# Kernel optimization log

Measured on AMD Instinct MI355X. Metric: run time of the kernel, lower is better.

## Reference

```python
import jax, jax.numpy as jnp
import numpy as np

N_HEADS = 16
N_CHANNELS = 1024
DIM_HEAD = N_CHANNELS // N_HEADS


def setup_inputs() -> dict:
    key = jax.random.key(0)
    k1, k2, k3, k4 = jax.random.split(key, 4)
    B, S, D = 4, 2048, N_CHANNELS
    x = jax.random.normal(k1, (B, S, D), dtype=jnp.float32)
    # in_proj: Linear(D, 3D, bias=False); torch weight shape [3D, D], y = x @ W.T
    w_in = jax.random.normal(k2, (3 * D, D), dtype=jnp.float32) * (1.0 / np.sqrt(D))
    # out_proj: Linear(D, D) with bias
    w_out = jax.random.normal(k3, (D, D), dtype=jnp.float32) * (1.0 / np.sqrt(D))
    b_out = jax.random.normal(k4, (D,), dtype=jnp.float32) * 0.01
    return {"x": x, "w_in": w_in, "w_out": w_out, "b_out": b_out}


def reference(x, w_in, w_out, b_out):
    B, S, D = x.shape
    H, Dh = N_HEADS, DIM_HEAD
    qkv = jnp.einsum('bsd,ed->bse', x, w_in)  # [B,S,3D]
    q, k, v = jnp.split(qkv, 3, axis=-1)
    # [B,S,D] -> [B,H,S,Dh]
    def to_heads(t):
        return t.reshape(B, S, H, Dh).transpose(0, 2, 1, 3)
    q, k, v = to_heads(q), to_heads(k), to_heads(v)
    scale = 1.0 / np.sqrt(Dh)
    scores = jnp.einsum('bhqd,bhkd->bhqk', q, k) * scale  # [B,H,S,S]
    attn = jax.nn.softmax(scores, axis=-1)
    out = jnp.einsum('bhqk,bhkd->bhqd', attn, v)  # [B,H,S,Dh]
    out = out.transpose(0, 2, 1, 3).reshape(B, S, D)
    return jnp.einsum('bsd,ed->bse', out, w_out) + b_out
```

## Files before the change

### kernel.cpp

```cpp
#include <hip/hip_runtime.h>

typedef __bf16 bf16;
typedef __bf16 bf16x2 __attribute__((ext_vector_type(2)));
typedef __bf16 bf16x4 __attribute__((ext_vector_type(4)));
typedef __bf16 bf16x8 __attribute__((ext_vector_type(8)));
typedef float f32x4 __attribute__((ext_vector_type(4)));

typedef __attribute__((address_space(1))) const unsigned int gq_t;
typedef __attribute__((address_space(3))) unsigned int lq_t;

__global__ __launch_bounds__(256) void cvt_bf16(const float* __restrict__ in,
                                                bf16* __restrict__ out,
                                                int n8) {
  int i = blockIdx.x * 256 + threadIdx.x;
  if (i >= n8) return;
  f32x4 a = ((const f32x4*)in)[2 * i];
  f32x4 b = ((const f32x4*)in)[2 * i + 1];
  bf16x8 o;
#pragma unroll
  for (int j = 0; j < 4; ++j) {
    o[j] = (bf16)a[j];
    o[4 + j] = (bf16)b[j];
  }
  ((bf16x8*)out)[i] = o;
}

template <typename TC, bool ADD_BIAS>
__global__ __launch_bounds__(256) void gemm_glds(const bf16* __restrict__ A,
                                                 const bf16* __restrict__ B,
                                                 const float* __restrict__ bias,
                                                 TC* __restrict__ C,
                                                 int M, int N, int K, int lda) {
  __shared__ __align__(16) bf16 As[128 * 64];
  __shared__ __align__(16) bf16 Bs[128 * 64];
  const int tid = threadIdx.x;
  const int lane = tid & 63;
  const int wid = tid >> 6;
  const int wr = wid >> 1, wc = wid & 1;
  const int m0 = blockIdx.y * 128;
  const int n0 = blockIdx.x * 128;
  const int l16 = lane & 15;
  const int lhi = lane >> 4;
  const int lr = lane >> 3;
  const int lc = (lane & 7) * 8;

  f32x4 acc[4][4] = {};

  for (int k0 = 0; k0 < K; k0 += 64) {
    __syncthreads();
#pragma unroll
    for (int i = 0; i < 4; ++i) {
      const int chunk = wid * 4 + i;
      const int row = chunk * 8 + lr;
      const bf16* ga = A + (size_t)(m0 + row) * lda + k0 + lc;
      const bf16* gb = B + (size_t)(n0 + row) * K + k0 + lc;
      __builtin_amdgcn_global_load_lds((gq_t*)ga, (lq_t*)&As[chunk * 512], 16,
                                       0, 0);
      __builtin_amdgcn_global_load_lds((gq_t*)gb, (lq_t*)&Bs[chunk * 512], 16,
                                       0, 0);
    }
    __syncthreads();
#pragma unroll
    for (int ks = 0; ks < 2; ++ks) {
      bf16x8 af[4], bfr[4];
#pragma unroll
      for (int i = 0; i < 4; ++i) {
        af[i] = *(const bf16x8*)(&As[(wr * 64 + i * 16 + l16) * 64 + ks * 32 +
                                     lhi * 8]);
        bfr[i] = *(const bf16x8*)(&Bs[(wc * 64 + i * 16 + l16) * 64 + ks * 32 +
                                      lhi * 8]);
      }
#pragma unroll
      for (int i = 0; i < 4; ++i)
#pragma unroll
        for (int j = 0; j < 4; ++j)
          acc[i][j] = __builtin_amdgcn_mfma_f32_16x16x32_bf16(af[i], bfr[j],
                                                              acc[i][j], 0, 0, 0);
    }
  }

#pragma unroll
  for (int i = 0; i < 4; ++i) {
    int row_base = m0 + wr * 64 + i * 16 + lhi * 4;
#pragma unroll
    for (int j = 0; j < 4; ++j) {
      int col = n0 + wc * 64 + j * 16 + l16;
      float bv = ADD_BIAS ? bias[col] : 0.0f;
#pragma unroll
      for (int r = 0; r < 4; ++r) {
        float val = acc[i][j][r] + bv;
        if constexpr (__is_same(TC, float))
          C[(size_t)(row_base + r) * N + col] = val;
        else
          C[(size_t)(row_base + r) * N + col] = (bf16)val;
      }
    }
  }
}

template <typename TA, typename TC, bool ADD_BIAS>
__global__ __launch_bounds__(256) void gemm_bt(const TA* __restrict__ A,
                                               const float* __restrict__ B,
                                               const float* __restrict__ bias,
                                               TC* __restrict__ C,
                                               int M, int N, int K,
                                               int lda, int row0) {
  __shared__ __align__(16) bf16 As[128][72];
  __shared__ __align__(16) bf16 Bs[128][72];
  const int tid = threadIdx.x;
  const int lane = tid & 63;
  const int wid = tid >> 6;
  const int wr = wid >> 1, wc = wid & 1;
  const int m0 = blockIdx.y * 128;
  const int n0 = blockIdx.x * 128;
  const int l16 = lane & 15;
  const int lhi = lane >> 4;

  f32x4 acc[4][4] = {};

  for (int k0 = 0; k0 < K; k0 += 64) {
    __syncthreads();
#pragma unroll
    for (int p = 0; p < 8; ++p) {
      int v = tid + p * 256;
      int row = v >> 4;
      int kc = (v & 15) * 4;
      size_t ai = (size_t)(row0 + m0 + row) * lda + k0 + kc;
      size_t bi = (size_t)(n0 + row) * K + k0 + kc;
      bf16x4 ab, bb;
      if constexpr (__is_same(TA, float)) {
        f32x4 a4 = *(const f32x4*)((const float*)A + ai);
#pragma unroll
        for (int j = 0; j < 4; ++j) ab[j] = (bf16)a4[j];
      } else {
        ab = *(const bf16x4*)((const bf16*)A + ai);
      }
      f32x4 b4 = *(const f32x4*)(B + bi);
#pragma unroll
      for (int j = 0; j < 4; ++j) bb[j] = (bf16)b4[j];
      *(bf16x4*)(&As[row][kc]) = ab;
      *(bf16x4*)(&Bs[row][kc]) = bb;
    }
    __syncthreads();
#pragma unroll
    for (int ks = 0; ks < 2; ++ks) {
      bf16x8 af[4], bfr[4];
#pragma unroll
      for (int i = 0; i < 4; ++i) {
        af[i] = *(const bf16x8*)(&As[wr * 64 + i * 16 + l16][ks * 32 + lhi * 8]);
        bfr[i] = *(const bf16x8*)(&Bs[wc * 64 + i * 16 + l16][ks * 32 + lhi * 8]);
      }
#pragma unroll
      for (int i = 0; i < 4; ++i)
#pragma unroll
        for (int j = 0; j < 4; ++j)
          acc[i][j] = __builtin_amdgcn_mfma_f32_16x16x32_bf16(af[i], bfr[j],
                                                              acc[i][j], 0, 0, 0);
    }
  }

#pragma unroll
  for (int i = 0; i < 4; ++i) {
    int row_base = m0 + wr * 64 + i * 16 + lhi * 4;
#pragma unroll
    for (int j = 0; j < 4; ++j) {
      int col = n0 + wc * 64 + j * 16 + l16;
      float bv = ADD_BIAS ? bias[col] : 0.0f;
#pragma unroll
      for (int r = 0; r < 4; ++r) {
        float val = acc[i][j][r] + bv;
        if constexpr (__is_same(TC, float))
          C[(size_t)(row_base + r) * N + col] = val;
        else
          C[(size_t)(row_base + r) * N + col] = (bf16)val;
      }
    }
  }
}

__global__ __launch_bounds__(256) void attn_fwd(bf16* __restrict__ qkv) {
  constexpr int S = 2048, D3 = 3072;
  constexpr float SCL = 0.18033688011112042f;
  constexpr float THR = 11.5f;
  __shared__ __align__(16) bf16 Kt[2][64][72];
  __shared__ __align__(16) bf16 Vt[2][64][72];
  __shared__ __align__(16) bf16 Pq[4][16][72];

  const int tid = threadIdx.x;
  const int lane = tid & 63;
  const int wid = tid >> 6;
  const int l16 = lane & 15, lhi = lane >> 4;

  const int nwg = gridDim.x * gridDim.y;
  const int bid = blockIdx.y * 32 + blockIdx.x;
  const int swz = (bid & 7) * (nwg >> 3) + (bid >> 3);
  const int bh = swz >> 5;
  const int b = bh >> 4, h = bh & 15;
  const int q0 = (swz & 31) * 64 + wid * 16;

  bf16* base = qkv + (size_t)b * S * D3;
  bf16* qbase = base + h * 64;
  const bf16* kbase = base + 1024 + h * 64;
  const bf16* vbase = base + 2048 + h * 64;

  bf16x8 qf[2];
#pragma unroll
  for (int ks = 0; ks < 2; ++ks)
    qf[ks] = *(const bf16x8*)(qbase + (size_t)(q0 + l16) * D3 + ks * 32 + lhi * 8);

  float m_i = -1e30f;
  float l_part = 0.0f;
  f32x4 o[4] = {};

  const int kp = tid & 31, oc = tid >> 5;

  {
    bf16x8 k0 = *(const bf16x8*)(kbase + (size_t)(2 * kp) * D3 + oc * 8);
    bf16x8 k1 = *(const bf16x8*)(kbase + (size_t)(2 * kp + 1) * D3 + oc * 8);
    bf16x8 v0 = *(const bf16x8*)(vbase + (size_t)(2 * kp) * D3 + oc * 8);
    bf16x8 v1 = *(const bf16x8*)(vbase + (size_t)(2 * kp + 1) * D3 + oc * 8);
    *(bf16x8*)(&Kt[0][2 * kp][oc * 8]) = k0;
    *(bf16x8*)(&Kt[0][2 * kp + 1][oc * 8]) = k1;
#pragma unroll
    for (int j = 0; j < 8; ++j) {
      bf16x2 pr;
      pr[0] = v0[j];
      pr[1] = v1[j];
      *(bf16x2*)(&Vt[0][oc * 8 + j][2 * kp]) = pr;
    }
  }
  __syncthreads();

  for (int t = 0; t < S; t += 64) {
    const int cur = (t >> 6) & 1;
    const bool havenext = (t + 64 < S);

    bf16x8 kn0, kn1, vn0, vn1;
    if (havenext) {
      const bf16* kb = kbase + (size_t)(t + 64) * D3;
      const bf16* vb = vbase + (size_t)(t + 64) * D3;
      kn0 = *(const bf16x8*)(kb + (size_t)(2 * kp) * D3 + oc * 8);
      kn1 = *(const bf16x8*)(kb + (size_t)(2 * kp + 1) * D3 + oc * 8);
      vn0 = *(const bf16x8*)(vb + (size_t)(2 * kp) * D3 + oc * 8);
      vn1 = *(const bf16x8*)(vb + (size_t)(2 * kp + 1) * D3 + oc * 8);
    }

    f32x4 sc[4] = {};
    __builtin_amdgcn_s_setprio(1);
#pragma unroll
    for (int ct = 0; ct < 4; ++ct) {
#pragma unroll
      for (int ks = 0; ks < 2; ++ks) {
        bf16x8 kf = *(const bf16x8*)(&Kt[cur][ct * 16 + l16][ks * 32 + lhi * 8]);
        sc[ct] = __builtin_amdgcn_mfma_f32_16x16x32_bf16(kf, qf[ks], sc[ct], 0, 0, 0);
      }
    }
    __builtin_amdgcn_s_setprio(0);

    float cm[4];
#pragma unroll
    for (int ct = 0; ct < 4; ++ct)
      cm[ct] = fmaxf(fmaxf(sc[ct][0], sc[ct][1]), fmaxf(sc[ct][2], sc[ct][3]));
    float mxs = fmaxf(fmaxf(cm[0], cm[1]), fmaxf(cm[2], cm[3])) * SCL;

    if (!__all(mxs - m_i <= THR)) {
      float mw = mxs;
      mw = fmaxf(mw, __shfl_xor(mw, 16));
      mw = fmaxf(mw, __shfl_xor(mw, 32));
      float nm = fmaxf(m_i, mw);
      float alpha = __builtin_amdgcn_exp2f(m_i - nm);
      m_i = nm;
      l_part *= alpha;
#pragma unroll
      for (int dt = 0; dt < 4; ++dt)
#pragma unroll
        for (int r = 0; r < 4; ++r) o[dt][r] *= alpha;
    }

    if (havenext) {
      *(bf16x8*)(&Kt[cur ^ 1][2 * kp][oc * 8]) = kn0;
      *(bf16x8*)(&Kt[cur ^ 1][2 * kp + 1][oc * 8]) = kn1;
#pragma unroll
      for (int j = 0; j < 8; ++j) {
        bf16x2 pr;
        pr[0] = vn0[j];
        pr[1] = vn1[j];
        *(bf16x2*)(&Vt[cur ^ 1][oc * 8 + j][2 * kp]) = pr;
      }
    }

    float rs4[4];
#pragma unroll
    for (int ct = 0; ct < 4; ++ct) {
#pragma unroll
      for (int r = 0; r < 4; ++r) {
        float p = __builtin_amdgcn_exp2f(__builtin_fmaf(sc[ct][r], SCL, -m_i));
        sc[ct][r] = p;
      }
      rs4[ct] = (sc[ct][0] + sc[ct][1]) + (sc[ct][2] + sc[ct][3]);
    }
    l_part += (rs4[0] + rs4[1]) + (rs4[2] + rs4[3]);

#pragma unroll
    for (int ct = 0; ct < 4; ++ct) {
      bf16x4 pk;
#pragma unroll
      for (int r = 0; r < 4; ++r) pk[r] = (bf16)sc[ct][r];
      *(bf16x4*)(&Pq[wid][l16][ct * 16 + lhi * 4]) = pk;
    }
    bf16x8 pf0 = *(const bf16x8*)(&Pq[wid][l16][lhi * 8]);
    bf16x8 pf1 = *(const bf16x8*)(&Pq[wid][l16][32 + lhi * 8]);

    __builtin_amdgcn_s_setprio(1);
#pragma unroll
    for (int dt = 0; dt < 4; ++dt) {
      bf16x8 vf0 = *(const bf16x8*)(&Vt[cur][dt * 16 + l16][lhi * 8]);
      bf16x8 vf1 = *(const bf16x8*)(&Vt[cur][dt * 16 + l16][32 + lhi * 8]);
      o[dt] = __builtin_amdgcn_mfma_f32_16x16x32_bf16(vf0, pf0, o[dt], 0, 0, 0);
      o[dt] = __builtin_amdgcn_mfma_f32_16x16x32_bf16(vf1, pf1, o[dt], 0, 0, 0);
    }
    __builtin_amdgcn_s_setprio(0);

    __syncthreads();
  }

  float l_i = l_part;
  l_i += __shfl_xor(l_i, 16);
  l_i += __shfl_xor(l_i, 32);
  float rl = 1.0f / l_i;
#pragma unroll
  for (int dt = 0; dt < 4; ++dt) {
    bf16x4 ok;
#pragma unroll
    for (int r = 0; r < 4; ++r) ok[r] = (bf16)(o[dt][r] * rl);
    *(bf16x4*)(&Pq[wid][l16][dt * 16 + lhi * 4]) = ok;
  }
  bf16x8 r0 = *(const bf16x8*)(&Pq[wid][l16][lhi * 16]);
  bf16x8 r1 = *(const bf16x8*)(&Pq[wid][l16][lhi * 16 + 8]);
  bf16* orow = qbase + (size_t)(q0 + l16) * D3 + lhi * 16;
  *(bf16x8*)(orow) = r0;
  *(bf16x8*)(orow + 8) = r1;
}

extern "C" void kernel_launch(void* const* d_in, const int* in_sizes, int n_in,
                              void* d_out, int out_size, void* d_ws,
                              size_t ws_size, hipStream_t stream) {
  constexpr int B = 4, S = 2048, D = 1024;

  const float* x = nullptr;
  const float* w_in = nullptr;
  const float* w_out = nullptr;
  const float* b_out = nullptr;
  for (int i = 0; i < n_in; ++i) {
    switch (in_sizes[i]) {
      case 8388608: x = (const float*)d_in[i]; break;
      case 3145728: w_in = (const float*)d_in[i]; break;
      case 1048576: w_out = (const float*)d_in[i]; break;
      case 1024: b_out = (const float*)d_in[i]; break;
    }
  }
  float* out = (float*)d_out;

  bf16* qkv = (bf16*)d_ws;
  const size_t need_full = (size_t)B * S * 3 * D * 2;
  const size_t need_cvt = need_full +
                          ((size_t)B * S * D +
                           (size_t)3 * D * D +
                           (size_t)D * D) * 2;

  if (ws_size >= need_cvt) {
    bf16* xb = qkv + (size_t)B * S * 3 * D;
    bf16* w_inb = xb + (size_t)B * S * D;
    bf16* w_outb = w_inb + (size_t)3 * D * D;
    const int nx8 = B * S * D / 8;
    const int nwi8 = 3 * D * D / 8;
    const int nwo8 = D * D / 8;
    cvt_bf16<<<dim3((nx8 + 255) / 256), 256, 0, stream>>>(x, xb, nx8);
    cvt_bf16<<<dim3((nwi8 + 255) / 256), 256, 0, stream>>>(w_in, w_inb, nwi8);
    cvt_bf16<<<dim3((nwo8 + 255) / 256), 256, 0, stream>>>(w_out, w_outb, nwo8);

    gemm_glds<bf16, false><<<dim3(3 * D / 128, B * S / 128), 256, 0, stream>>>(
        xb, w_inb, nullptr, qkv, B * S, 3 * D, D, D);
    attn_fwd<<<dim3(S / 64, B * 16), 256, 0, stream>>>(qkv);
    gemm_glds<float, true><<<dim3(D / 128, B * S / 128), 256, 0, stream>>>(
        qkv, w_outb, b_out, out, B * S, D, D, 3 * D);
  } else if (ws_size >= need_full) {
    gemm_bt<float, bf16, false><<<dim3(3 * D / 128, B * S / 128), 256, 0,
                                  stream>>>(x, w_in, nullptr, qkv, B * S,
                                            3 * D, D, D, 0);
    attn_fwd<<<dim3(S / 64, B * 16), 256, 0, stream>>>(qkv);
    gemm_bt<bf16, float, true><<<dim3(D / 128, B * S / 128), 256, 0, stream>>>(
        qkv, w_out, b_out, out, B * S, D, D, 3 * D, 0);
  } else {
    for (int b0 = 0; b0 < B; ++b0) {
      gemm_bt<float, bf16, false><<<dim3(3 * D / 128, S / 128), 256, 0,
                                    stream>>>(x, w_in, nullptr, qkv, S, 3 * D,
                                              D, D, b0 * S);
      attn_fwd<<<dim3(S / 64, 16), 256, 0, stream>>>(qkv);
      gemm_bt<bf16, float, true><<<dim3(D / 128, S / 128), 256, 0, stream>>>(
          qkv, w_out, b_out, out + (size_t)b0 * S * D, S, D, D, 3 * D, 0);
    }
  }
}
```

Baseline: 356.1 us.

## Process two 16-row query tiles per wave in attention to reuse K/V tiles

Each wave now handles 32 query rows (two independent 16-row tiles with separate softmax state), so each workgroup covers 128 queries and the grid is halved. K and V tiles loaded into shared memory, and the K/V fragments read from it, are reused across twice as many queries, cutting global and LDS traffic per query. In exchange it roughly doubles accumulator and score registers, which may lower occupancy, and halves the number of workgroups (1024 instead of 2048).

```diff
diff --git a/kernel.cpp b/kernel.cpp
--- a/kernel.cpp
+++ b/kernel.cpp
@@ -192,25 +192,27 @@
   const int l16 = lane & 15, lhi = lane >> 4;
 
   const int nwg = gridDim.x * gridDim.y;
-  const int bid = blockIdx.y * 32 + blockIdx.x;
+  const int bid = blockIdx.y * gridDim.x + blockIdx.x;
   const int swz = (bid & 7) * (nwg >> 3) + (bid >> 3);
-  const int bh = swz >> 5;
+  const int bh = swz >> 4;
   const int b = bh >> 4, h = bh & 15;
-  const int q0 = (swz & 31) * 64 + wid * 16;
+  const int q0 = (swz & 15) * 128 + wid * 32;
 
   bf16* base = qkv + (size_t)b * S * D3;
   bf16* qbase = base + h * 64;
   const bf16* kbase = base + 1024 + h * 64;
   const bf16* vbase = base + 2048 + h * 64;
 
-  bf16x8 qf[2];
-#pragma unroll
-  for (int ks = 0; ks < 2; ++ks)
-    qf[ks] = *(const bf16x8*)(qbase + (size_t)(q0 + l16) * D3 + ks * 32 + lhi * 8);
-
-  float m_i = -1e30f;
-  float l_part = 0.0f;
-  f32x4 o[4] = {};
+  bf16x8 qfA[2], qfB[2];
+#pragma unroll
+  for (int ks = 0; ks < 2; ++ks) {
+    qfA[ks] = *(const bf16x8*)(qbase + (size_t)(q0 + l16) * D3 + ks * 32 + lhi * 8);
+    qfB[ks] = *(const bf16x8*)(qbase + (size_t)(q0 + 16 + l16) * D3 + ks * 32 + lhi * 8);
+  }
+
+  float mA = -1e30f, mB = -1e30f;
+  float lA = 0.0f, lB = 0.0f;
+  f32x4 oA[4] = {}, oB[4] = {};
 
   const int kp = tid & 31, oc = tid >> 5;
 
@@ -245,37 +247,100 @@
       vn1 = *(const bf16x8*)(vb + (size_t)(2 * kp + 1) * D3 + oc * 8);
     }
 
-    f32x4 sc[4] = {};
+    f32x4 scA[4] = {}, scB[4] = {};
     __builtin_amdgcn_s_setprio(1);
 #pragma unroll
     for (int ct = 0; ct < 4; ++ct) {
 #pragma unroll
       for (int ks = 0; ks < 2; ++ks) {
         bf16x8 kf = *(const bf16x8*)(&Kt[cur][ct * 16 + l16][ks * 32 + lhi * 8]);
-        sc[ct] = __builtin_amdgcn_mfma_f32_16x16x32_bf16(kf, qf[ks], sc[ct], 0, 0, 0);
+        scA[ct] = __builtin_amdgcn_mfma_f32_16x16x32_bf16(kf, qfA[ks], scA[ct], 0, 0, 0);
+        scB[ct] = __builtin_amdgcn_mfma_f32_16x16x32_bf16(kf, qfB[ks], scB[ct], 0, 0, 0);
       }
     }
     __builtin_amdgcn_s_setprio(0);
 
-    float cm[4];
-#pragma unroll
-    for (int ct = 0; ct < 4; ++ct)
-      cm[ct] = fmaxf(fmaxf(sc[ct][0], sc[ct][1]), fmaxf(sc[ct][2], sc[ct][3]));
-    float mxs = fmaxf(fmaxf(cm[0], cm[1]), fmaxf(cm[2], cm[3])) * SCL;
-
-    if (!__all(mxs - m_i <= THR)) {
-      float mw = mxs;
-      mw = fmaxf(mw, __shfl_xor(mw, 16));
-      mw = fmaxf(mw, __shfl_xor(mw, 32));
-      float nm = fmaxf(m_i, mw);
-      float alpha = __builtin_amdgcn_exp2f(m_i - nm);
-      m_i = nm;
-      l_part *= alpha;
-#pragma unroll
-      for (int dt = 0; dt < 4; ++dt)
-#pragma unroll
-        for (int r = 0; r < 4; ++r) o[dt][r] *= alpha;
-    }
+    {
+      float cm[4];
+#pragma unroll
+      for (int ct = 0; ct < 4; ++ct)
+        cm[ct] = fmaxf(fmaxf(scA[ct][0], scA[ct][1]), fmaxf(scA[ct][2], scA[ct][3]));
+      float mxs = fmaxf(fmaxf(cm[0], cm[1]), fmaxf(cm[2], cm[3])) * SCL;
+      if (!__all(mxs - mA <= THR)) {
+        float mw = mxs;
+        mw = fmaxf(mw, __shfl_xor(mw, 16));
+        mw = fmaxf(mw, __shfl_xor(mw, 32));
+        float nm = fmaxf(mA, mw);
+        float alpha = __builtin_amdgcn_exp2f(mA - nm);
+        mA = nm;
+        lA *= alpha;
+#pragma unroll
+        for (int dt = 0; dt < 4; ++dt)
+#pragma unroll
+          for (int r = 0; r < 4; ++r) oA[dt][r] *= alpha;
+      }
+      float rs4[4];
+#pragma unroll
+      for (int ct = 0; ct < 4; ++ct) {
+#pragma unroll
+        for (int r = 0; r < 4; ++r) {
+          float p = __builtin_amdgcn_exp2f(__builtin_fmaf(scA[ct][r], SCL, -mA));
+          scA[ct][r] = p;
+        }
+        rs4[ct] = (scA[ct][0] + scA[ct][1]) + (scA[ct][2] + scA[ct][3]);
+      }
+      lA += (rs4[0] + rs4[1]) + (rs4[2] + rs4[3]);
+    }
+#pragma unroll
+    for (int ct = 0; ct < 4; ++ct) {
+      bf16x4 pk;
+#pragma unroll
+      for (int r = 0; r < 4; ++r) pk[r] = (bf16)scA[ct][r];
+      *(bf16x4*)(&Pq[wid][l16][ct * 16 + lhi * 4]) = pk;
+    }
+    bf16x8 pfA0 = *(const bf16x8*)(&Pq[wid][l16][lhi * 8]);
+    bf16x8 pfA1 = *(const bf16x8*)(&Pq[wid][l16][32 + lhi * 8]);
+
+    {
+      float cm[4];
+#pragma unroll
+      for (int ct = 0; ct < 4; ++ct)
+        cm[ct] = fmaxf(fmaxf(scB[ct][0], scB[ct][1]), fmaxf(scB[ct][2], scB[ct][3]));
+      float mxs = fmaxf(fmaxf(cm[0], cm[1]), fmaxf(cm[2], cm[3])) * SCL;
+      if (!__all(mxs - mB <= THR)) {
+        float mw = mxs;
+        mw = fmaxf(mw, __shfl_xor(mw, 16));
+        mw = fmaxf(mw, __shfl_xor(mw, 32));
+        float nm = fmaxf(mB, mw);
+        float alpha = __builtin_amdgcn_exp2f(mB - nm);
+        mB = nm;
+        lB *= alpha;
+#pragma unroll
+        for (int dt = 0; dt < 4; ++dt)
+#pragma unroll
+          for (int r = 0; r < 4; ++r) oB[dt][r] *= alpha;
+      }
+      float rs4[4];
+#pragma unroll
+      for (int ct = 0; ct < 4; ++ct) {
+#pragma unroll
+        for (int r = 0; r < 4; ++r) {
+          float p = __builtin_amdgcn_exp2f(__builtin_fmaf(scB[ct][r], SCL, -mB));
+          scB[ct][r] = p;
+        }
+        rs4[ct] = (scB[ct][0] + scB[ct][1]) + (scB[ct][2] + scB[ct][3]);
+      }
+      lB += (rs4[0] + rs4[1]) + (rs4[2] + rs4[3]);
+    }
+#pragma unroll
+    for (int ct = 0; ct < 4; ++ct) {
+      bf16x4 pk;
+#pragma unroll
+      for (int r = 0; r < 4; ++r) pk[r] = (bf16)scB[ct][r];
+      *(bf16x4*)(&Pq[wid][l16][ct * 16 + lhi * 4]) = pk;
+    }
+    bf16x8 pfB0 = *(const bf16x8*)(&Pq[wid][l16][lhi * 8]);
+    bf16x8 pfB1 = *(const bf16x8*)(&Pq[wid][l16][32 + lhi * 8]);
 
     if (havenext) {
       *(bf16x8*)(&Kt[cur ^ 1][2 * kp][oc * 8]) = kn0;
@@ -289,57 +354,57 @@
       }
     }
 
-    float rs4[4];
-#pragma unroll
-    for (int ct = 0; ct < 4; ++ct) {
-#pragma unroll
-      for (int r = 0; r < 4; ++r) {
-        float p = __builtin_amdgcn_exp2f(__builtin_fmaf(sc[ct][r], SCL, -m_i));
-        sc[ct][r] = p;
-      }
-      rs4[ct] = (sc[ct][0] + sc[ct][1]) + (sc[ct][2] + sc[ct][3]);
-    }
-    l_part += (rs4[0] + rs4[1]) + (rs4[2] + rs4[3]);
-
-#pragma unroll
-    for (int ct = 0; ct < 4; ++ct) {
-      bf16x4 pk;
-#pragma unroll
-      for (int r = 0; r < 4; ++r) pk[r] = (bf16)sc[ct][r];
-      *(bf16x4*)(&Pq[wid][l16][ct * 16 + lhi * 4]) = pk;
-    }
-    bf16x8 pf0 = *(const bf16x8*)(&Pq[wid][l16][lhi * 8]);
-    bf16x8 pf1 = *(const bf16x8*)(&Pq[wid][l16][32 + lhi * 8]);
-
     __builtin_amdgcn_s_setprio(1);
 #pragma unroll
     for (int dt = 0; dt < 4; ++dt) {
       bf16x8 vf0 = *(const bf16x8*)(&Vt[cur][dt * 16 + l16][lhi * 8]);
       bf16x8 vf1 = *(const bf16x8*)(&Vt[cur][dt * 16 + l16][32 + lhi * 8]);
-      o[dt] = __builtin_amdgcn_mfma_f32_16x16x32_bf16(vf0, pf0, o[dt], 0, 0, 0);
-      o[dt] = __builtin_amdgcn_mfma_f32_16x16x32_bf16(vf1, pf1, o[dt], 0, 0, 0);
+      oA[dt] = __builtin_amdgcn_mfma_f32_16x16x32_bf16(vf0, pfA0, oA[dt], 0, 0, 0);
+      oA[dt] = __builtin_amdgcn_mfma_f32_16x16x32_bf16(vf1, pfA1, oA[dt], 0, 0, 0);
+      oB[dt] = __builtin_amdgcn_mfma_f32_16x16x32_bf16(vf0, pfB0, oB[dt], 0, 0, 0);
+      oB[dt] = __builtin_amdgcn_mfma_f32_16x16x32_bf16(vf1, pfB1, oB[dt], 0, 0, 0);
     }
     __builtin_amdgcn_s_setprio(0);
 
     __syncthreads();
   }
 
-  float l_i = l_part;
-  l_i += __shfl_xor(l_i, 16);
-  l_i += __shfl_xor(l_i, 32);
-  float rl = 1.0f / l_i;
-#pragma unroll
-  for (int dt = 0; dt < 4; ++dt) {
-    bf16x4 ok;
-#pragma unroll
-    for (int r = 0; r < 4; ++r) ok[r] = (bf16)(o[dt][r] * rl);
-    *(bf16x4*)(&Pq[wid][l16][dt * 16 + lhi * 4]) = ok;
-  }
-  bf16x8 r0 = *(const bf16x8*)(&Pq[wid][l16][lhi * 16]);
-  bf16x8 r1 = *(const bf16x8*)(&Pq[wid][l16][lhi * 16 + 8]);
-  bf16* orow = qbase + (size_t)(q0 + l16) * D3 + lhi * 16;
-  *(bf16x8*)(orow) = r0;
-  *(bf16x8*)(orow + 8) = r1;
+  {
+    float l_i = lA;
+    l_i += __shfl_xor(l_i, 16);
+    l_i += __shfl_xor(l_i, 32);
+    float rl = 1.0f / l_i;
+#pragma unroll
+    for (int dt = 0; dt < 4; ++dt) {
+      bf16x4 ok;
+#pragma unroll
+      for (int r = 0; r < 4; ++r) ok[r] = (bf16)(oA[dt][r] * rl);
+      *(bf16x4*)(&Pq[wid][l16][dt * 16 + lhi * 4]) = ok;
+    }
+    bf16x8 r0 = *(const bf16x8*)(&Pq[wid][l16][lhi * 16]);
+    bf16x8 r1 = *(const bf16x8*)(&Pq[wid][l16][lhi * 16 + 8]);
+    bf16* orow = qbase + (size_t)(q0 + l16) * D3 + lhi * 16;
+    *(bf16x8*)(orow) = r0;
+    *(bf16x8*)(orow + 8) = r1;
+  }
+  {
+    float l_i = lB;
+    l_i += __shfl_xor(l_i, 16);
+    l_i += __shfl_xor(l_i, 32);
+    float rl = 1.0f / l_i;
+#pragma unroll
+    for (int dt = 0; dt < 4; ++dt) {
+      bf16x4 ok;
+#pragma unroll
+      for (int r = 0; r < 4; ++r) ok[r] = (bf16)(oB[dt][r] * rl);
+      *(bf16x4*)(&Pq[wid][l16][dt * 16 + lhi * 4]) = ok;
+    }
+    bf16x8 r0 = *(const bf16x8*)(&Pq[wid][l16][lhi * 16]);
+    bf16x8 r1 = *(const bf16x8*)(&Pq[wid][l16][lhi * 16 + 8]);
+    bf16* orow = qbase + (size_t)(q0 + 16 + l16) * D3 + lhi * 16;
+    *(bf16x8*)(orow) = r0;
+    *(bf16x8*)(orow + 8) = r1;
+  }
 }
 
 extern "C" void kernel_launch(void* const* d_in, const int* in_sizes, int n_in,
@@ -381,14 +446,14 @@
 
     gemm_glds<bf16, false><<<dim3(3 * D / 128, B * S / 128), 256, 0, stream>>>(
         xb, w_inb, nullptr, qkv, B * S, 3 * D, D, D);
-    attn_fwd<<<dim3(S / 64, B * 16), 256, 0, stream>>>(qkv);
+    attn_fwd<<<dim3(S / 128, B * 16), 256, 0, stream>>>(qkv);
     gemm_glds<float, true><<<dim3(D / 128, B * S / 128), 256, 0, stream>>>(
         qkv, w_outb, b_out, out, B * S, D, D, 3 * D);
   } else if (ws_size >= need_full) {
     gemm_bt<float, bf16, false><<<dim3(3 * D / 128, B * S / 128), 256, 0,
                                   stream>>>(x, w_in, nullptr, qkv, B * S,
                                             3 * D, D, D, 0);
-    attn_fwd<<<dim3(S / 64, B * 16), 256, 0, stream>>>(qkv);
+    attn_fwd<<<dim3(S / 128, B * 16), 256, 0, stream>>>(qkv);
     gemm_bt<bf16, float, true><<<dim3(D / 128, B * S / 128), 256, 0, stream>>>(
         qkv, w_out, b_out, out, B * S, D, D, 3 * D, 0);
   } else {
@@ -396,7 +461,7 @@
       gemm_bt<float, bf16, false><<<dim3(3 * D / 128, S / 128), 256, 0,
                                     stream>>>(x, w_in, nullptr, qkv, S, 3 * D,
                                               D, D, b0 * S);
-      attn_fwd<<<dim3(S / 64, 16), 256, 0, stream>>>(qkv);
+      attn_fwd<<<dim3(S / 128, 16), 256, 0, stream>>>(qkv);
       gemm_bt<bf16, float, true><<<dim3(D / 128, S / 128), 256, 0, stream>>>(
           qkv, w_out, b_out, out + (size_t)b0 * S * D, S, D, D, 3 * D, 0);
     }
```

Result: faster. 328.2 us (-7.8%).

## Process four query subtiles per wave to reuse K/V tiles in attention

Applied to the files above, without the earlier changes.

Each wave now handles 64 query rows (four 16-row subtiles) instead of 16, so a workgroup covers 256 queries and the grid shrinks by four. Every K/V tile loaded into shared memory and every K/V fragment read from LDS now feeds four times as many MFMAs, which cuts global K/V traffic and LDS reads per unit of work. The cost is far more registers per thread (four sets of Q fragments, output accumulators and P fragments), which lowers occupancy. The grid also drops to 512 workgroups, which may underfill the GPU.

```diff
diff --git a/kernel.cpp b/kernel.cpp
--- a/kernel.cpp
+++ b/kernel.cpp
@@ -192,25 +192,28 @@
   const int l16 = lane & 15, lhi = lane >> 4;
 
   const int nwg = gridDim.x * gridDim.y;
-  const int bid = blockIdx.y * 32 + blockIdx.x;
+  const int bid = blockIdx.y * gridDim.x + blockIdx.x;
   const int swz = (bid & 7) * (nwg >> 3) + (bid >> 3);
-  const int bh = swz >> 5;
+  const int bh = swz >> 3;
   const int b = bh >> 4, h = bh & 15;
-  const int q0 = (swz & 31) * 64 + wid * 16;
+  const int q0 = (swz & 7) * 256 + wid * 64;
 
   bf16* base = qkv + (size_t)b * S * D3;
   bf16* qbase = base + h * 64;
   const bf16* kbase = base + 1024 + h * 64;
   const bf16* vbase = base + 2048 + h * 64;
 
-  bf16x8 qf[2];
-#pragma unroll
-  for (int ks = 0; ks < 2; ++ks)
-    qf[ks] = *(const bf16x8*)(qbase + (size_t)(q0 + l16) * D3 + ks * 32 + lhi * 8);
-
-  float m_i = -1e30f;
-  float l_part = 0.0f;
-  f32x4 o[4] = {};
+  bf16x8 qf[4][2];
+#pragma unroll
+  for (int s = 0; s < 4; ++s)
+#pragma unroll
+    for (int ks = 0; ks < 2; ++ks)
+      qf[s][ks] = *(const bf16x8*)(qbase + (size_t)(q0 + s * 16 + l16) * D3 +
+                                   ks * 32 + lhi * 8);
+
+  float m_i[4] = {-1e30f, -1e30f, -1e30f, -1e30f};
+  float l_p[4] = {};
+  f32x4 o[4][4] = {};
 
   const int kp = tid & 31, oc = tid >> 5;
 
@@ -245,36 +248,70 @@
       vn1 = *(const bf16x8*)(vb + (size_t)(2 * kp + 1) * D3 + oc * 8);
     }
 
-    f32x4 sc[4] = {};
-    __builtin_amdgcn_s_setprio(1);
-#pragma unroll
-    for (int ct = 0; ct < 4; ++ct) {
-#pragma unroll
-      for (int ks = 0; ks < 2; ++ks) {
-        bf16x8 kf = *(const bf16x8*)(&Kt[cur][ct * 16 + l16][ks * 32 + lhi * 8]);
-        sc[ct] = __builtin_amdgcn_mfma_f32_16x16x32_bf16(kf, qf[ks], sc[ct], 0, 0, 0);
-      }
-    }
-    __builtin_amdgcn_s_setprio(0);
-
-    float cm[4];
-#pragma unroll
-    for (int ct = 0; ct < 4; ++ct)
-      cm[ct] = fmaxf(fmaxf(sc[ct][0], sc[ct][1]), fmaxf(sc[ct][2], sc[ct][3]));
-    float mxs = fmaxf(fmaxf(cm[0], cm[1]), fmaxf(cm[2], cm[3])) * SCL;
-
-    if (!__all(mxs - m_i <= THR)) {
-      float mw = mxs;
-      mw = fmaxf(mw, __shfl_xor(mw, 16));
-      mw = fmaxf(mw, __shfl_xor(mw, 32));
-      float nm = fmaxf(m_i, mw);
-      float alpha = __builtin_amdgcn_exp2f(m_i - nm);
-      m_i = nm;
-      l_part *= alpha;
-#pragma unroll
-      for (int dt = 0; dt < 4; ++dt)
-#pragma unroll
-        for (int r = 0; r < 4; ++r) o[dt][r] *= alpha;
+    bf16x8 pf[4][2];
+
+#pragma unroll
+    for (int p = 0; p < 2; ++p) {
+      f32x4 sc[2][4] = {};
+      __builtin_amdgcn_s_setprio(1);
+#pragma unroll
+      for (int ct = 0; ct < 4; ++ct) {
+#pragma unroll
+        for (int ks = 0; ks < 2; ++ks) {
+          bf16x8 kf = *(const bf16x8*)(&Kt[cur][ct * 16 + l16][ks * 32 + lhi * 8]);
+          sc[0][ct] = __builtin_amdgcn_mfma_f32_16x16x32_bf16(
+              kf, qf[2 * p][ks], sc[0][ct], 0, 0, 0);
+          sc[1][ct] = __builtin_amdgcn_mfma_f32_16x16x32_bf16(
+              kf, qf[2 * p + 1][ks], sc[1][ct], 0, 0, 0);
+        }
+      }
+      __builtin_amdgcn_s_setprio(0);
+
+#pragma unroll
+      for (int j = 0; j < 2; ++j) {
+        const int s = 2 * p + j;
+        float cm[4];
+#pragma unroll
+        for (int ct = 0; ct < 4; ++ct)
+          cm[ct] = fmaxf(fmaxf(sc[j][ct][0], sc[j][ct][1]),
+                         fmaxf(sc[j][ct][2], sc[j][ct][3]));
+        float mxs = fmaxf(fmaxf(cm[0], cm[1]), fmaxf(cm[2], cm[3])) * SCL;
+        if (!__all(mxs - m_i[s] <= THR)) {
+          float mw = mxs;
+          mw = fmaxf(mw, __shfl_xor(mw, 16));
+          mw = fmaxf(mw, __shfl_xor(mw, 32));
+          float nm = fmaxf(m_i[s], mw);
+          float alpha = __builtin_amdgcn_exp2f(m_i[s] - nm);
+          m_i[s] = nm;
+          l_p[s] *= alpha;
+#pragma unroll
+          for (int dt = 0; dt < 4; ++dt)
+#pragma unroll
+            for (int r = 0; r < 4; ++r) o[s][dt][r] *= alpha;
+        }
+        float rs4[4];
+#pragma unroll
+        for (int ct = 0; ct < 4; ++ct) {
+#pragma unroll
+          for (int r = 0; r < 4; ++r) {
+            float pv = __builtin_amdgcn_exp2f(
+                __builtin_fmaf(sc[j][ct][r], SCL, -m_i[s]));
+            sc[j][ct][r] = pv;
+          }
+          rs4[ct] = (sc[j][ct][0] + sc[j][ct][1]) + (sc[j][ct][2] + sc[j][ct][3]);
+        }
+        l_p[s] += (rs4[0] + rs4[1]) + (rs4[2] + rs4[3]);
+
+#pragma unroll
+        for (int ct = 0; ct < 4; ++ct) {
+          bf16x4 pk;
+#pragma unroll
+          for (int r = 0; r < 4; ++r) pk[r] = (bf16)sc[j][ct][r];
+          *(bf16x4*)(&Pq[wid][l16][ct * 16 + lhi * 4]) = pk;
+        }
+        pf[s][0] = *(const bf16x8*)(&Pq[wid][l16][lhi * 8]);
+        pf[s][1] = *(const bf16x8*)(&Pq[wid][l16][32 + lhi * 8]);
+      }
     }
 
     if (havenext) {
@@ -289,57 +326,43 @@
       }
     }
 
-    float rs4[4];
-#pragma unroll
-    for (int ct = 0; ct < 4; ++ct) {
-#pragma unroll
-      for (int r = 0; r < 4; ++r) {
-        float p = __builtin_amdgcn_exp2f(__builtin_fmaf(sc[ct][r], SCL, -m_i));
-        sc[ct][r] = p;
-      }
-      rs4[ct] = (sc[ct][0] + sc[ct][1]) + (sc[ct][2] + sc[ct][3]);
-    }
-    l_part += (rs4[0] + rs4[1]) + (rs4[2] + rs4[3]);
-
-#pragma unroll
-    for (int ct = 0; ct < 4; ++ct) {
-      bf16x4 pk;
-#pragma unroll
-      for (int r = 0; r < 4; ++r) pk[r] = (bf16)sc[ct][r];
-      *(bf16x4*)(&Pq[wid][l16][ct * 16 + lhi * 4]) = pk;
-    }
-    bf16x8 pf0 = *(const bf16x8*)(&Pq[wid][l16][lhi * 8]);
-    bf16x8 pf1 = *(const bf16x8*)(&Pq[wid][l16][32 + lhi * 8]);
-
     __builtin_amdgcn_s_setprio(1);
 #pragma unroll
     for (int dt = 0; dt < 4; ++dt) {
       bf16x8 vf0 = *(const bf16x8*)(&Vt[cur][dt * 16 + l16][lhi * 8]);
       bf16x8 vf1 = *(const bf16x8*)(&Vt[cur][dt * 16 + l16][32 + lhi * 8]);
-      o[dt] = __builtin_amdgcn_mfma_f32_16x16x32_bf16(vf0, pf0, o[dt], 0, 0, 0);
-      o[dt] = __builtin_amdgcn_mfma_f32_16x16x32_bf16(vf1, pf1, o[dt], 0, 0, 0);
+#pragma unroll
+      for (int s = 0; s < 4; ++s) {
+        o[s][dt] = __builtin_amdgcn_mfma_f32_16x16x32_bf16(vf0, pf[s][0],
+                                                           o[s][dt], 0, 0, 0);
+        o[s][dt] = __builtin_amdgcn_mfma_f32_16x16x32_bf16(vf1, pf[s][1],
+                                                           o[s][dt], 0, 0, 0);
+      }
     }
     __builtin_amdgcn_s_setprio(0);
 
     __syncthreads();
   }
 
-  float l_i = l_part;
-  l_i += __shfl_xor(l_i, 16);
-  l_i += __shfl_xor(l_i, 32);
-  float rl = 1.0f / l_i;
-#pragma unroll
-  for (int dt = 0; dt < 4; ++dt) {
-    bf16x4 ok;
-#pragma unroll
-    for (int r = 0; r < 4; ++r) ok[r] = (bf16)(o[dt][r] * rl);
-    *(bf16x4*)(&Pq[wid][l16][dt * 16 + lhi * 4]) = ok;
-  }
-  bf16x8 r0 = *(const bf16x8*)(&Pq[wid][l16][lhi * 16]);
-  bf16x8 r1 = *(const bf16x8*)(&Pq[wid][l16][lhi * 16 + 8]);
-  bf16* orow = qbase + (size_t)(q0 + l16) * D3 + lhi * 16;
-  *(bf16x8*)(orow) = r0;
-  *(bf16x8*)(orow + 8) = r1;
+#pragma unroll
+  for (int s = 0; s < 4; ++s) {
+    float l_i = l_p[s];
+    l_i += __shfl_xor(l_i, 16);
+    l_i += __shfl_xor(l_i, 32);
+    float rl = 1.0f / l_i;
+#pragma unroll
+    for (int dt = 0; dt < 4; ++dt) {
+      bf16x4 ok;
+#pragma unroll
+      for (int r = 0; r < 4; ++r) ok[r] = (bf16)(o[s][dt][r] * rl);
+      *(bf16x4*)(&Pq[wid][l16][dt * 16 + lhi * 4]) = ok;
+    }
+    bf16x8 r0 = *(const bf16x8*)(&Pq[wid][l16][lhi * 16]);
+    bf16x8 r1 = *(const bf16x8*)(&Pq[wid][l16][lhi * 16 + 8]);
+    bf16* orow = qbase + (size_t)(q0 + s * 16 + l16) * D3 + lhi * 16;
+    *(bf16x8*)(orow) = r0;
+    *(bf16x8*)(orow + 8) = r1;
+  }
 }
 
 extern "C" void kernel_launch(void* const* d_in, const int* in_sizes, int n_in,
@@ -381,14 +404,14 @@
 
     gemm_glds<bf16, false><<<dim3(3 * D / 128, B * S / 128), 256, 0, stream>>>(
         xb, w_inb, nullptr, qkv, B * S, 3 * D, D, D);
-    attn_fwd<<<dim3(S / 64, B * 16), 256, 0, stream>>>(qkv);
+    attn_fwd<<<dim3(S / 256, B * 16), 256, 0, stream>>>(qkv);
     gemm_glds<float, true><<<dim3(D / 128, B * S / 128), 256, 0, stream>>>(
         qkv, w_outb, b_out, out, B * S, D, D, 3 * D);
   } else if (ws_size >= need_full) {
     gemm_bt<float, bf16, false><<<dim3(3 * D / 128, B * S / 128), 256, 0,
                                   stream>>>(x, w_in, nullptr, qkv, B * S,
                                             3 * D, D, D, 0);
-    attn_fwd<<<dim3(S / 64, B * 16), 256, 0, stream>>>(qkv);
+    attn_fwd<<<dim3(S / 256, B * 16), 256, 0, stream>>>(qkv);
     gemm_bt<bf16, float, true><<<dim3(D / 128, B * S / 128), 256, 0, stream>>>(
         qkv, w_out, b_out, out, B * S, D, D, 3 * D, 0);
   } else {
@@ -396,7 +419,7 @@
       gemm_bt<float, bf16, false><<<dim3(3 * D / 128, S / 128), 256, 0,
                                     stream>>>(x, w_in, nullptr, qkv, S, 3 * D,
                                               D, D, b0 * S);
-      attn_fwd<<<dim3(S / 64, 16), 256, 0, stream>>>(qkv);
+      attn_fwd<<<dim3(S / 256, 16), 256, 0, stream>>>(qkv);
       gemm_bt<bf16, float, true><<<dim3(D / 128, S / 128), 256, 0, stream>>>(
           qkv, w_out, b_out, out + (size_t)b0 * S * D, S, D, D, 3 * D, 0);
     }
```

New measurement: 344.6 us. 1.03x faster.
